# Kernel tuning notes

Measured on AMD Instinct MI355X. Metric: run time of the kernel, lower is better.

The kernel has to match this reference:

```python
import jax, jax.numpy as jnp
import numpy as np
import itertools
from itertools import combinations

N_QUBITS = 6
DIM = 2 ** N_QUBITS            # 64
N_GEN = DIM ** 2 - 1           # 4095 (SU(2^n) generators)
K_LOCAL = 2
OBS_DIM = 2 ** K_LOCAL         # 4
WIRE_GROUPS = [list(c) for c in combinations(range(N_QUBITS), K_LOCAL)]
N_OBS = len(WIRE_GROUPS)       # 15
N_OFF = OBS_DIM * (OBS_DIM - 1) // 2  # 6
CHUNK_DIM = 512
T_EMB = 256
HID = 256
BATCH = 512

# lower-triangle (i>j) flat ordering used by create_Hermitian: c = i*(i-1)/2 + j
_TRI_R = np.array([i for i in range(1, OBS_DIM) for j in range(i)])
_TRI_C = np.array([j for i in range(1, OBS_DIM) for j in range(i)])
_DIAG = np.arange(OBS_DIM - 1)  # diag slots 0..N-2 get 2*D[1..N-1]; last diag is 0


def _pauli_basis():
    """Lexicographic Pauli words on N_QUBITS qubits, identity excluded -> (N_GEN, DIM, DIM)."""
    I = np.eye(2, dtype=np.complex64)
    X = np.array([[0, 1], [1, 0]], dtype=np.complex64)
    Y = np.array([[0, -1j], [1j, 0]], dtype=np.complex64)
    Z = np.array([[1, 0], [0, -1]], dtype=np.complex64)
    P1 = {'I': I, 'X': X, 'Y': Y, 'Z': Z}
    out = np.empty((N_GEN, DIM, DIM), dtype=np.complex64)
    k = 0
    for word in itertools.product('IXYZ', repeat=N_QUBITS):
        if all(c == 'I' for c in word):
            continue
        m = np.array([[1.0 + 0j]], dtype=np.complex64)
        for c in word:
            m = np.kron(m, P1[c])
        out[k] = m
        k += 1
    return jnp.asarray(out)


def setup_inputs() -> dict:
    key = jax.random.key(0)
    ks = jax.random.split(key, 12)
    inp = {
        'x': jax.random.normal(ks[0], (BATCH, CHUNK_DIM + T_EMB), dtype=jnp.float32),
        # enc_proj: Linear(768,256) -> SiLU -> Linear(256,4095)
        'W1': jax.random.normal(ks[1], (CHUNK_DIM + T_EMB, HID), dtype=jnp.float32) * 0.02,
        'b1': jnp.zeros((HID,), dtype=jnp.float32),
        'W2': jax.random.normal(ks[2], (HID, N_GEN), dtype=jnp.float32) * 0.02,
        'b2': jnp.zeros((N_GEN,), dtype=jnp.float32),
        # ANO Hermitian params (std=2.0 per torch init)
        'Aoff': jax.random.normal(ks[3], (N_OBS, N_OFF), dtype=jnp.float32) * 2.0,
        'Boff': jax.random.normal(ks[4], (N_OBS, N_OFF), dtype=jnp.float32) * 2.0,
        'Ddiag': jax.random.normal(ks[5], (N_OBS, OBS_DIM), dtype=jnp.float32) * 2.0,
        # vel_head: Linear(15,256) -> SiLU -> Linear(256,512)
        'Wv1': jax.random.normal(ks[6], (N_OBS, HID), dtype=jnp.float32) * 0.02,
        'bv1': jnp.zeros((HID,), dtype=jnp.float32),
        'Wv2': jax.random.normal(ks[7], (HID, CHUNK_DIM), dtype=jnp.float32) * 0.02,
        'bv2': jnp.zeros((CHUNK_DIM,), dtype=jnp.float32),
        'pauli': _pauli_basis(),  # fixed SU(2^n) generator basis (constant)
    }
    return inp


def _build_H(Aoff, Boff, Ddiag):
    """Batched create_Hermitian: (N_OBS, 4, 4) complex. h + h^H semantics."""
    H = jnp.zeros((N_OBS, OBS_DIM, OBS_DIM), dtype=jnp.complex64)
    off = Aoff.astype(jnp.complex64) + 1j * Boff.astype(jnp.complex64)
    H = H.at[:, _TRI_R, _TRI_C].set(off)
    H = H + jnp.conj(jnp.swapaxes(H, -1, -2))
    H = H.at[:, _DIAG, _DIAG].set((2.0 * Ddiag[:, 1:]).astype(jnp.complex64))
    return H


def _forward(x, W1, b1, W2, b2, Aoff, Boff, Ddiag, Wv1, bv1, Wv2, bv2, pauli):
    B = x.shape[0]
    # enc_proj MLP -> SU(2^n) angles theta (B, 4095)
    enc = jax.nn.silu(x @ W1 + b1) @ W2 + b2
    # SpecialUnitary: U = exp(i * sum_m theta_m P_m); apply to |0...0> via eigh of the
    # Hermitian effective generator H_eff = sum_m theta_m P_m.
    H_eff = jnp.einsum('bm,mij->bij', enc.astype(jnp.complex64), pauli)  # (B, 64, 64)
    lam, V = jnp.linalg.eigh(H_eff)
    # psi = V @ diag(exp(i*lam)) @ V^dag @ e0 ; (V^dag e0)_j = conj(V[0, j])
    psi = jnp.einsum('bij,bj->bi', V, jnp.exp(1j * lam.astype(jnp.complex64)) * jnp.conj(V[:, 0, :]))
    H = _build_H(Aoff, Boff, Ddiag)  # (15, 4, 4)
    psi_t = psi.reshape((B,) + (2,) * N_QUBITS)
    q = []
    for w, (a, b) in enumerate(WIRE_GROUPS):
        # bring wires (a,b) to front (wire order: first wire is most significant bit)
        pg = jnp.moveaxis(psi_t, (1 + a, 1 + b), (1, 2)).reshape(B, OBS_DIM, -1)
        # <H> = tr(rho H), rho_kl = sum_r psi[k,r] conj(psi[l,r])
        q.append(jnp.einsum('bkr,blr,lk->b', pg, jnp.conj(pg), H[w]).real)
    q = jnp.stack(q, axis=1).astype(jnp.float32)  # (B, 15)
    return jax.nn.silu(q @ Wv1 + bv1) @ Wv2 + bv2  # (B, 512)


def reference(x, W1, b1, W2, b2, Aoff, Boff, Ddiag, Wv1, bv1, Wv2, bv2, pauli):
    return _forward(x, W1, b1, W2, b2, Aoff, Boff, Ddiag, Wv1, bv1, Wv2, bv2, pauli)
```

## Files before the change

### kernel.cpp

```cpp
#include <hip/hip_runtime.h>
#include <hip/hip_bf16.h>

#define BATCH   512
#define INDIM   768
#define HID     256
#define NGEN    4095
#define NOBS    15
#define OUTDIM  512
#define DIM     64

typedef __hip_bfloat16 bf16;

__device__ int      g_isf32;
__device__ float    g_theta[(size_t)BATCH*NGEN];
__device__ float    g_q[BATCH*NOBS];

__device__ __forceinline__ float tof(bf16 v){ return __bfloat162float(v); }
__device__ __forceinline__ float silu(float x){ return x / (1.f + __expf(-x)); }
__device__ __forceinline__ float blo(unsigned u){ return __uint_as_float(u<<16); }
__device__ __forceinline__ float bhi(unsigned u){ return __uint_as_float(u & 0xFFFF0000u); }

template<bool F32>
__device__ __forceinline__ float LD(const void* p, size_t i){
  if(F32) return ((const float*)p)[i];
  else    return tof(((const bf16*)p)[i]);
}

__device__ __forceinline__ unsigned spread6(unsigned x){
  return (x&1u) | ((x&2u)<<1) | ((x&4u)<<2) | ((x&8u)<<3) | ((x&16u)<<4) | ((x&32u)<<5);
}

__constant__ int c_WA[15] = {0,0,0,0,0,1,1,1,1,2,2,2,3,3,4};
__constant__ int c_WB[15] = {1,2,3,4,5,2,3,4,5,3,4,5,4,5,5};
__constant__ int c_Lt[6]  = {1,2,2,3,3,3};
__constant__ int c_Kt[6]  = {0,0,1,0,1,2};

__global__ __launch_bounds__(256) void k_detect(const unsigned* __restrict__ w1raw){
  __shared__ int sh[256];
  const int t = threadIdx.x;
  int c = 0;
  for(int i=t;i<1024;i+=256){
    unsigned ub = (w1raw[i]>>8) & 0x7Fu;
    if(ub>=0x30u && ub<=0x3Fu) c++;
  }
  sh[t] = c;
  __syncthreads();
  for(int s=128;s>0;s>>=1){
    if(t<s) sh[t] += sh[t+s];
    __syncthreads();
  }
  if(t==0) g_isf32 = (sh[0] < 512) ? 1 : 0;
}

template<bool F32>
__device__ void enc_body(const void* __restrict__ x, const void* __restrict__ W1,
                         const void* __restrict__ b1, const void* __restrict__ W2,
                         const void* __restrict__ b2,
                         float (*xl_t)[4], float (*hl_t)[4]){
  const int t  = threadIdx.x;
  const int b0 = (blockIdx.x >> 3) * 4;
  const int c0 = (blockIdx.x & 7) * 512;

  #pragma unroll
  for(int r=0;r<4;r++)
    for(int k=t;k<INDIM;k+=256) xl_t[k][r] = LD<F32>(x,(size_t)(b0+r)*INDIM+k);
  __syncthreads();

  {
    float acc1[4]={0.f,0.f,0.f,0.f};
    for(int k0=0;k0<INDIM;k0+=8){
      float wv[8];
      #pragma unroll
      for(int u=0;u<8;u++) wv[u] = LD<F32>(W1,(size_t)(k0+u)*HID+t);
      #pragma unroll
      for(int u=0;u<8;u++){
        float4 xa = *(const float4*)&xl_t[k0+u][0];
        float w = wv[u];
        acc1[0]+=xa.x*w; acc1[1]+=xa.y*w; acc1[2]+=xa.z*w; acc1[3]+=xa.w*w;
      }
    }
    float bb = LD<F32>(b1,t);
    #pragma unroll
    for(int r=0;r<4;r++) hl_t[t][r] = silu(acc1[r]+bb);
  }
  __syncthreads();

  const int colA = c0 + t;
  const int colB = c0 + 256 + t;
  const bool okB = (colB < NGEN);
  float acc[4][2];
  {
    float bva = LD<F32>(b2,colA);
    float bvb = okB ? LD<F32>(b2,colB) : 0.f;
    #pragma unroll
    for(int r=0;r<4;r++){ acc[r][0]=bva; acc[r][1]=bvb; }
  }
  for(int k0=0;k0<HID;k0+=8){
    float wa[8], wb[8];
    #pragma unroll
    for(int u=0;u<8;u++){
      wa[u] = LD<F32>(W2,(size_t)(k0+u)*NGEN + colA);
      wb[u] = okB ? LD<F32>(W2,(size_t)(k0+u)*NGEN + colB) : 0.f;
    }
    #pragma unroll
    for(int u=0;u<8;u++){
      float4 ha = *(const float4*)&hl_t[k0+u][0];
      float fa = wa[u], fb = wb[u];
      acc[0][0]+=ha.x*fa; acc[0][1]+=ha.x*fb;
      acc[1][0]+=ha.y*fa; acc[1][1]+=ha.y*fb;
      acc[2][0]+=ha.z*fa; acc[2][1]+=ha.z*fb;
      acc[3][0]+=ha.w*fa; acc[3][1]+=ha.w*fb;
    }
  }
  #pragma unroll
  for(int r=0;r<4;r++){
    g_theta[(size_t)(b0+r)*NGEN + colA] = acc[r][0];
    if(okB) g_theta[(size_t)(b0+r)*NGEN + colB] = acc[r][1];
  }
}

__global__ __launch_bounds__(256) void k_enc(const void* x,const void* W1,const void* b1,
                                             const void* W2,const void* b2){
  __shared__ __align__(16) float xl_t[INDIM][4];
  __shared__ __align__(16) float hl_t[HID][4];
  if(g_isf32) enc_body<true >(x,W1,b1,W2,b2,xl_t,hl_t);
  else        enc_body<false>(x,W1,b1,W2,b2,xl_t,hl_t);
}

template<bool F32>
__device__ void state_body(const void* __restrict__ Aoff, const void* __restrict__ Boff,
                           const void* __restrict__ Ddiag,
                           const void* __restrict__ Wv1, const void* __restrict__ bv1,
                           const void* __restrict__ Wv2, const void* __restrict__ bv2,
                           void* __restrict__ out, char* sm){
  float*  th   = (float*)sm;
  float*  HH   = (float*)(sm + 16384);
  typedef float2 rep_t[66];
  rep_t*  vrA  = (rep_t*)sm;
  rep_t*  vrB  = (rep_t*)(sm + 2112);
  float2* ps   = (float2*)(sm + 4224);
  float2* coef = (float2*)(sm + 4736);
  float*  rs   = (float*)(sm + 6016);
  float*  qacc = (float*)(sm + 6272);
  float*  s_inva = (float*)(sm + 6336);
  int*    s_K    = (int*)(sm + 6340);
  float*  s_aG   = (float*)(sm + 6344);
  float*  hl   = (float*)(sm + 6400);
  float (*part)[64][8] = (float(*)[64][8])(sm + 7424);
  float*  n11  = (float*)(sm + 15616);
  float*  n12  = (float*)(sm + 15872);

  const int b = blockIdx.x, t = threadIdx.x;
  for(int m=t;m<NGEN;m+=256) th[m] = g_theta[(size_t)b*NGEN+m];
  __syncthreads();

  const int lane = t & 63, wav = t >> 6;
  for(int it=0; it<16; ++it){
    int d = (it<<2) | wav;
    unsigned td = (unsigned)(lane & d);
    unsigned tn = (unsigned)(lane & ~d) & 63u;
    unsigned w  = spread6((unsigned)d) + spread6(td) + 3u*spread6(tn);
    float thv = (w==0u) ? 0.f : th[w-1u];
    int ny = __popc(td) & 3;
    float gr = (ny==0)?  thv : (ny==2 ? -thv : 0.f);
    float gi = (ny==1)? -thv : (ny==3 ?  thv : 0.f);
    #pragma unroll
    for(int s=1;s<64;s<<=1){
      float pr = __shfl_xor(gr, s);
      float pi = __shfl_xor(gi, s);
      if(lane & s){ gr = pr - gr; gi = pi - gi; }
      else        { gr = gr + pr; gi = gi + pi; }
    }
    int j = lane ^ d;
    HH[lane*132 + 2*j]   = gr;
    HH[lane*132 + 2*j+1] = gi;
  }
  __syncthreads();

  const int i = t >> 2, c = t & 3, j0 = c*16;
  float hreg[32];
  float rsum = 0.f;
  #pragma unroll
  for(int jj=0;jj<16;jj+=2){
    float4 hv = *(const float4*)&HH[i*132 + 2*(j0+jj)];
    hreg[2*jj+0]=hv.x; hreg[2*jj+1]=hv.y; hreg[2*jj+2]=hv.z; hreg[2*jj+3]=hv.w;
    rsum += fabsf(hv.x)+fabsf(hv.y)+fabsf(hv.z)+fabsf(hv.w);
  }
  rsum += __shfl_xor(rsum,1);
  rsum += __shfl_xor(rsum,2);
  if(c==0) rs[i] = rsum;
  __syncthreads();

  if(t==0){
    float aG = 0.5f;
    for(int r=0;r<DIM;r++) aG = fmaxf(aG, rs[r]);
    *s_aG = aG;
  }
  __syncthreads();
  const float aG    = *s_aG;
  const float invaG = 1.f/aG;

  {
    rep_t* pv1 = vrA;
    rep_t* pv0 = vrB;
    if(t < DIM){
      float2 e0v = make_float2(t==0?1.f:0.f, 0.f);
      #pragma unroll
      for(int cc=0;cc<4;cc++) pv1[cc][t] = e0v;
    }
    __syncthreads();
    for(int m=1;m<=12;++m){
      const float* vb = (const float*)&pv1[c][0];
      float yr=0.f, yi=0.f;
      #pragma unroll
      for(int jj=0;jj<16;jj+=2){
        float4 xv = *(const float4*)&vb[2*(j0+jj)];
        float hr0=hreg[2*jj], hi0=hreg[2*jj+1], hr1=hreg[2*jj+2], hi1=hreg[2*jj+3];
        yr += hr0*xv.x - hi0*xv.y;
        yi += hr0*xv.y + hi0*xv.x;
        yr += hr1*xv.z - hi1*xv.w;
        yi += hr1*xv.w + hi1*xv.z;
      }
      yr += __shfl_xor(yr,1); yr += __shfl_xor(yr,2);
      yi += __shfl_xor(yi,1); yi += __shfl_xor(yi,2);
      if(c==0){
        float vnr = invaG*yr, vni = invaG*yi;
        float2 vn = make_float2(vnr, vni);
        #pragma unroll
        for(int cc=0;cc<4;cc++) pv0[cc][i] = vn;
        if(m==11) n11[i] = vnr*vnr + vni*vni;
        if(m==12) n12[i] = vnr*vnr + vni*vni;
      }
      __syncthreads();
      rep_t* tmp = pv0; pv0 = pv1; pv1 = tmp;
    }
  }

  if(t==0){
    float s11=0.f, s12=0.f;
    for(int r=0;r<DIM;r++){ s11 += n11[r]; s12 += n12[r]; }
    float a = aG;
    if(s11 > 1e-30f){
      float ratio = sqrtf(s12/s11);
      float ap = 1.35f * ratio * aG;
      a = fminf(aG, fmaxf(ap, 0.5f));
    }
    int K = (int)ceilf(a + 6.f*cbrtf(a) + 10.f);
    if(K>150) K=150;
    float bkp=0.f, bk=1e-35f, snorm=0.f;
    for(int k=K+12;k>=1;--k){
      float bkm = (2.f*(float)k/a)*bk - bkp;
      int n = k-1;
      if(n<=K) coef[n].x = bkm;
      if((n&1)==0) snorm += (n==0?1.f:2.f)*bkm;
      bkp = bk; bk = bkm;
    }
    float invs = 1.f/snorm;
    for(int n=0;n<=K;n++){
      float cv = coef[n].x*invs*(n==0?1.f:2.f);
      int p = n&3;
      float cr = (p==0)? cv : (p==2 ? -cv : 0.f);
      float ci = (p==1)? cv : (p==3 ? -cv : 0.f);
      coef[n] = make_float2(cr,ci);
    }
    *s_K = K;
    *s_inva = 1.f/a;
  }
  __syncthreads();
  const float inva = *s_inva;
  const int K = *s_K;

  rep_t* v0r = vrA;
  rep_t* v1r = vrB;
  if(t < DIM){
    float2 w1 = make_float2(HH[t*132+0]*inva, HH[t*132+1]*inva);
    float2 e0 = make_float2(t==0?1.f:0.f, 0.f);
    #pragma unroll
    for(int cc=0;cc<4;cc++){ v0r[cc][t] = e0; v1r[cc][t] = w1; }
    float2 c0 = coef[0], c1 = coef[1];
    float2 p;
    p.x = (t==0?c0.x:0.f) + c1.x*w1.x - c1.y*w1.y;
    p.y = (t==0?c0.y:0.f) + c1.x*w1.y + c1.y*w1.x;
    ps[t] = p;
  }
  __syncthreads();

  for(int k=2;k<=K;k++){
    const float* vb = (const float*)&v1r[c][0];
    float yr=0.f, yi=0.f;
    #pragma unroll
    for(int jj=0;jj<16;jj+=2){
      float4 xv = *(const float4*)&vb[2*(j0+jj)];
      float hr0=hreg[2*jj], hi0=hreg[2*jj+1], hr1=hreg[2*jj+2], hi1=hreg[2*jj+3];
      yr += hr0*xv.x - hi0*xv.y;
      yi += hr0*xv.y + hi0*xv.x;
      yr += hr1*xv.z - hi1*xv.w;
      yi += hr1*xv.w + hi1*xv.z;
    }
    yr += __shfl_xor(yr,1); yr += __shfl_xor(yr,2);
    yi += __shfl_xor(yi,1); yi += __shfl_xor(yi,2);
    if(c==0){
      float2 vm = v0r[0][i];
      float2 vn = make_float2(2.f*inva*yr - vm.x, 2.f*inva*yi - vm.y);
      #pragma unroll
      for(int cc=0;cc<4;cc++) v0r[cc][i] = vn;
      float2 ck = coef[k];
      float2 p = ps[i];
      p.x += ck.x*vn.x - ck.y*vn.y;
      p.y += ck.x*vn.y + ck.y*vn.x;
      ps[i] = p;
    }
    __syncthreads();
    rep_t* tmp = v0r; v0r = v1r; v1r = tmp;
  }

  if(t<NOBS) qacc[t]=0.f;
  __syncthreads();

  if(t<150){
    int w = t/10, s = t%10;
    int posA = 5 - c_WA[w], posB = 5 - c_WB[w];
    float contrib = 0.f;
    bool have = false;
    if(s<4){
      int kk = s;
      if(kk<3){
        float val = 0.f;
        for(int r=0;r<16;r++){
          int idx = (((kk>>1)&1)<<posA) | ((kk&1)<<posB);
          int rb = 3;
          #pragma unroll
          for(int p=5;p>=0;--p){
            if(p==posA || p==posB) continue;
            idx |= ((r>>rb)&1)<<p;
            rb--;
          }
          float2 pv = ps[idx];
          val += pv.x*pv.x + pv.y*pv.y;
        }
        contrib = val*2.f*LD<F32>(Ddiag, w*4 + kk + 1);
        have = true;
      }
    } else {
      int cc = s-4;
      int l = c_Lt[cc], kk = c_Kt[cc];
      float zr=0.f, zi=0.f;
      for(int r=0;r<16;r++){
        int idxk = (((kk>>1)&1)<<posA) | ((kk&1)<<posB);
        int idxl = (((l >>1)&1)<<posA) | ((l &1)<<posB);
        int rb = 3;
        #pragma unroll
        for(int p=5;p>=0;--p){
          if(p==posA || p==posB) continue;
          int bit = (r>>rb)&1;
          idxk |= bit<<p; idxl |= bit<<p;
          rb--;
        }
        float2 pk = ps[idxk], pl = ps[idxl];
        zr += pk.x*pl.x + pk.y*pl.y;
        zi += pk.y*pl.x - pk.x*pl.y;
      }
      contrib = 2.f*(zr*LD<F32>(Aoff,w*6+cc) - zi*LD<F32>(Boff,w*6+cc));
      have = true;
    }
    if(have) atomicAdd(&qacc[w], contrib);
  }
  __syncthreads();
  if(t<NOBS) g_q[(size_t)b*NOBS + t] = qacc[t];

  if(!F32){
    {
      float acc = tof(((const bf16*)bv1)[t]);
      #pragma unroll
      for(int k=0;k<NOBS;k++) acc += qacc[k]*tof(((const bf16*)Wv1)[k*HID+t]);
      hl[t] = silu(acc);
    }
    __syncthreads();
    const int rg = t >> 6;
    const uint4* w2v = (const uint4*)Wv2;
    float a8[8] = {0.f,0.f,0.f,0.f,0.f,0.f,0.f,0.f};
    for(int kk=0; kk<64; kk+=8){
      uint4 wv[8];
      #pragma unroll
      for(int u=0;u<8;u++) wv[u] = w2v[(size_t)(rg*64+kk+u)*64 + lane];
      #pragma unroll
      for(int u=0;u<8;u++){
        float hk = hl[rg*64+kk+u];
        a8[0] += hk*blo(wv[u].x); a8[1] += hk*bhi(wv[u].x);
        a8[2] += hk*blo(wv[u].y); a8[3] += hk*bhi(wv[u].y);
        a8[4] += hk*blo(wv[u].z); a8[5] += hk*bhi(wv[u].z);
        a8[6] += hk*blo(wv[u].w); a8[7] += hk*bhi(wv[u].w);
      }
    }
    #pragma unroll
    for(int j=0;j<8;j++) part[rg][lane][j] = a8[j];
    __syncthreads();
    {
      int cA = 2*t, cB = 2*t+1;
      float vA = tof(((const bf16*)bv2)[cA]);
      float vB = tof(((const bf16*)bv2)[cB]);
      #pragma unroll
      for(int r2=0;r2<4;r2++){
        vA += part[r2][cA>>3][cA&7];
        vB += part[r2][cB>>3][cB&7];
      }
      bf16 ha = __float2bfloat16(vA), hb = __float2bfloat16(vB);
      unsigned pw = (unsigned)(*(unsigned short*)&ha) |
                    ((unsigned)(*(unsigned short*)&hb)<<16);
      ((unsigned*)out)[(size_t)b*(OUTDIM/2) + t] = pw;
    }
  }
}

__global__ __launch_bounds__(256) void k_state(const void* Aoff,const void* Boff,const void* Dd,
                                               const void* Wv1,const void* bv1,
                                               const void* Wv2,const void* bv2, void* out){
  __shared__ __align__(16) char sm[50176];
  if(g_isf32) state_body<true >(Aoff,Boff,Dd,Wv1,bv1,Wv2,bv2,out,sm);
  else        state_body<false>(Aoff,Boff,Dd,Wv1,bv1,Wv2,bv2,out,sm);
}

template<bool F32>
__device__ void vel_body(const void* __restrict__ Wv1, const void* __restrict__ bv1,
                         const void* __restrict__ Wv2, const void* __restrict__ bv2,
                         void* __restrict__ out){
  const int b = blockIdx.x, t = threadIdx.x;
  if(F32){
    __shared__ float ql[NOBS];
    __shared__ float hl[HID];
    if(t<NOBS) ql[t] = g_q[(size_t)b*NOBS+t];
    __syncthreads();
    float acc = LD<F32>(bv1,t);
    #pragma unroll
    for(int k=0;k<NOBS;k++) acc += ql[k]*LD<F32>(Wv1,k*HID+t);
    hl[t] = silu(acc);
    __syncthreads();
    #pragma unroll
    for(int oo=0;oo<2;oo++){
      int o = t + oo*256;
      float s0=0.f;
      for(int k=0;k<HID;k++) s0 += hl[k]*LD<F32>(Wv2,(size_t)k*OUTDIM+o);
      ((float*)out)[(size_t)b*OUTDIM+o] = LD<F32>(bv2,o) + s0;
    }
  }
}

__global__ __launch_bounds__(256) void k_vel(const void* Wv1,const void* bv1,
                                             const void* Wv2,const void* bv2, void* out){
  if(g_isf32) vel_body<true >(Wv1,bv1,Wv2,bv2,out);
  else        vel_body<false>(Wv1,bv1,Wv2,bv2,out);
}

extern "C" void kernel_launch(void* const* d_in, const int* in_sizes, int n_in,
                              void* d_out, int out_size, void* d_ws, size_t ws_size,
                              hipStream_t stream){
  const void* x    = d_in[0];
  const void* W1   = d_in[1];
  const void* b1   = d_in[2];
  const void* W2   = d_in[3];
  const void* b2   = d_in[4];
  const void* Aoff = d_in[5];
  const void* Boff = d_in[6];
  const void* Dd   = d_in[7];
  const void* Wv1  = d_in[8];
  const void* bv1  = d_in[9];
  const void* Wv2  = d_in[10];
  const void* bv2  = d_in[11];

  k_detect<<<1,256,0,stream>>>((const unsigned*)W1);
  k_enc  <<<1024,256,0,stream>>>(x,W1,b1,W2,b2);
  k_state<<<BATCH,256,0,stream>>>(Aoff,Boff,Dd,Wv1,bv1,Wv2,bv2,d_out);
  k_vel  <<<BATCH,256,0,stream>>>(Wv1,bv1,Wv2,bv2,d_out);
}
```

Baseline: 266.8 us.

## Split encoder into pack, layer-1 and layer-2 kernels with padded fp32 weights

The fused encoder kernel is replaced by three launches. The first converts inputs and weights to fp32 and pads NGEN to 4096. The second computes the hidden layer once per 4 rows, so it is no longer recomputed by each of the 8 column blocks. The third computes the output layer with 8 rows per block and float4-vectorised, padded loads and stores. This removes the 8x redundant layer-1 work and the unaligned W2 accesses, at the cost of extra launches and a per-call conversion pass over all weights (about 4 MB for W2).

```diff
diff --git a/kernel.cpp b/kernel.cpp
--- a/kernel.cpp
+++ b/kernel.cpp
@@ -5,6 +5,7 @@
 #define INDIM   768
 #define HID     256
 #define NGEN    4095
+#define NGENP   4096
 #define NOBS    15
 #define OUTDIM  512
 #define DIM     64
@@ -12,8 +13,14 @@
 typedef __hip_bfloat16 bf16;
 
 __device__ int      g_isf32;
-__device__ float    g_theta[(size_t)BATCH*NGEN];
+__device__ float    g_theta[(size_t)BATCH*NGENP];
 __device__ float    g_q[BATCH*NOBS];
+__device__ float    g_h[(size_t)BATCH*HID];
+__device__ float    g_xp[(size_t)BATCH*INDIM];
+__device__ float    g_W1p[(size_t)INDIM*HID];
+__device__ float    g_b1p[HID];
+__device__ float    g_W2p[(size_t)HID*NGENP];
+__device__ float    g_b2p[NGENP];
 
 __device__ __forceinline__ float tof(bf16 v){ return __bfloat162float(v); }
 __device__ __forceinline__ float silu(float x){ return x / (1.f + __expf(-x)); }
@@ -53,78 +60,85 @@
 }
 
 template<bool F32>
-__device__ void enc_body(const void* __restrict__ x, const void* __restrict__ W1,
-                         const void* __restrict__ b1, const void* __restrict__ W2,
-                         const void* __restrict__ b2,
-                         float (*xl_t)[4], float (*hl_t)[4]){
+__device__ void pack_body(const void* __restrict__ x, const void* __restrict__ W1,
+                          const void* __restrict__ b1, const void* __restrict__ W2,
+                          const void* __restrict__ b2){
+  const size_t gid = (size_t)blockIdx.x*256 + threadIdx.x;
+  const size_t stride = (size_t)gridDim.x*256;
+  for(size_t i=gid;i<(size_t)BATCH*INDIM;i+=stride) g_xp[i]  = LD<F32>(x,i);
+  for(size_t i=gid;i<(size_t)INDIM*HID;i+=stride)   g_W1p[i] = LD<F32>(W1,i);
+  for(size_t i=gid;i<HID;i+=stride)                 g_b1p[i] = LD<F32>(b1,i);
+  for(size_t i=gid;i<(size_t)HID*NGENP;i+=stride){
+    size_t k = i>>12, c = i&4095;
+    g_W2p[i] = (c<NGEN) ? LD<F32>(W2,k*NGEN+c) : 0.f;
+  }
+  for(size_t i=gid;i<NGENP;i+=stride) g_b2p[i] = (i<NGEN) ? LD<F32>(b2,i) : 0.f;
+}
+
+__global__ __launch_bounds__(256) void k_pack(const void* x,const void* W1,const void* b1,
+                                              const void* W2,const void* b2){
+  if(g_isf32) pack_body<true >(x,W1,b1,W2,b2);
+  else        pack_body<false>(x,W1,b1,W2,b2);
+}
+
+__global__ __launch_bounds__(256) void k_enc1(){
+  __shared__ __align__(16) float xl[INDIM][4];
+  const int t = threadIdx.x, b0 = blockIdx.x*4;
+  for(int i=t;i<4*INDIM;i+=256){
+    int r = i/INDIM, k = i - r*INDIM;
+    xl[k][r] = g_xp[(size_t)(b0+r)*INDIM + k];
+  }
+  __syncthreads();
+  const int rh = t>>7, tc = t&127;
+  float a00=0.f,a01=0.f,a10=0.f,a11=0.f;
+  for(int k0=0;k0<INDIM;k0+=8){
+    #pragma unroll
+    for(int u=0;u<8;u++){
+      float2 wv = *(const float2*)&g_W1p[(size_t)(k0+u)*HID + 2*tc];
+      float2 xv = *(const float2*)&xl[k0+u][2*rh];
+      a00 += xv.x*wv.x; a01 += xv.x*wv.y;
+      a10 += xv.y*wv.x; a11 += xv.y*wv.y;
+    }
+  }
+  const float bb0 = g_b1p[2*tc], bb1 = g_b1p[2*tc+1];
+  g_h[(size_t)(b0+2*rh+0)*HID + 2*tc+0] = silu(a00+bb0);
+  g_h[(size_t)(b0+2*rh+0)*HID + 2*tc+1] = silu(a01+bb1);
+  g_h[(size_t)(b0+2*rh+1)*HID + 2*tc+0] = silu(a10+bb0);
+  g_h[(size_t)(b0+2*rh+1)*HID + 2*tc+1] = silu(a11+bb1);
+}
+
+__global__ __launch_bounds__(512) void k_enc2(){
+  __shared__ __align__(16) float hl[HID][8];
   const int t  = threadIdx.x;
-  const int b0 = (blockIdx.x >> 3) * 4;
-  const int c0 = (blockIdx.x & 7) * 512;
-
+  const int b0 = (blockIdx.x>>2)*8;
+  const int c0 = (blockIdx.x&3)*1024;
+  for(int i=t;i<8*HID;i+=512){
+    int r = i>>8, k = i&255;
+    hl[k][r] = g_h[(size_t)(b0+r)*HID + k];
+  }
+  __syncthreads();
+  const int rh = t>>8, tc = t&255;
+  const int col = c0 + 4*tc;
+  float4 bv = *(const float4*)&g_b2p[col];
+  float acc[4][4];
   #pragma unroll
-  for(int r=0;r<4;r++)
-    for(int k=t;k<INDIM;k+=256) xl_t[k][r] = LD<F32>(x,(size_t)(b0+r)*INDIM+k);
-  __syncthreads();
-
-  {
-    float acc1[4]={0.f,0.f,0.f,0.f};
-    for(int k0=0;k0<INDIM;k0+=8){
-      float wv[8];
-      #pragma unroll
-      for(int u=0;u<8;u++) wv[u] = LD<F32>(W1,(size_t)(k0+u)*HID+t);
-      #pragma unroll
-      for(int u=0;u<8;u++){
-        float4 xa = *(const float4*)&xl_t[k0+u][0];
-        float w = wv[u];
-        acc1[0]+=xa.x*w; acc1[1]+=xa.y*w; acc1[2]+=xa.z*w; acc1[3]+=xa.w*w;
-      }
-    }
-    float bb = LD<F32>(b1,t);
-    #pragma unroll
-    for(int r=0;r<4;r++) hl_t[t][r] = silu(acc1[r]+bb);
-  }
-  __syncthreads();
-
-  const int colA = c0 + t;
-  const int colB = c0 + 256 + t;
-  const bool okB = (colB < NGEN);
-  float acc[4][2];
-  {
-    float bva = LD<F32>(b2,colA);
-    float bvb = okB ? LD<F32>(b2,colB) : 0.f;
-    #pragma unroll
-    for(int r=0;r<4;r++){ acc[r][0]=bva; acc[r][1]=bvb; }
-  }
+  for(int i=0;i<4;i++){ acc[i][0]=bv.x; acc[i][1]=bv.y; acc[i][2]=bv.z; acc[i][3]=bv.w; }
   for(int k0=0;k0<HID;k0+=8){
-    float wa[8], wb[8];
     #pragma unroll
     for(int u=0;u<8;u++){
-      wa[u] = LD<F32>(W2,(size_t)(k0+u)*NGEN + colA);
-      wb[u] = okB ? LD<F32>(W2,(size_t)(k0+u)*NGEN + colB) : 0.f;
-    }
-    #pragma unroll
-    for(int u=0;u<8;u++){
-      float4 ha = *(const float4*)&hl_t[k0+u][0];
-      float fa = wa[u], fb = wb[u];
-      acc[0][0]+=ha.x*fa; acc[0][1]+=ha.x*fb;
-      acc[1][0]+=ha.y*fa; acc[1][1]+=ha.y*fb;
-      acc[2][0]+=ha.z*fa; acc[2][1]+=ha.z*fb;
-      acc[3][0]+=ha.w*fa; acc[3][1]+=ha.w*fb;
+      float4 wv = *(const float4*)&g_W2p[(size_t)(k0+u)*NGENP + col];
+      float4 hv = *(const float4*)&hl[k0+u][4*rh];
+      acc[0][0]+=hv.x*wv.x; acc[0][1]+=hv.x*wv.y; acc[0][2]+=hv.x*wv.z; acc[0][3]+=hv.x*wv.w;
+      acc[1][0]+=hv.y*wv.x; acc[1][1]+=hv.y*wv.y; acc[1][2]+=hv.y*wv.z; acc[1][3]+=hv.y*wv.w;
+      acc[2][0]+=hv.z*wv.x; acc[2][1]+=hv.z*wv.y; acc[2][2]+=hv.z*wv.z; acc[2][3]+=hv.z*wv.w;
+      acc[3][0]+=hv.w*wv.x; acc[3][1]+=hv.w*wv.y; acc[3][2]+=hv.w*wv.z; acc[3][3]+=hv.w*wv.w;
     }
   }
   #pragma unroll
-  for(int r=0;r<4;r++){
-    g_theta[(size_t)(b0+r)*NGEN + colA] = acc[r][0];
-    if(okB) g_theta[(size_t)(b0+r)*NGEN + colB] = acc[r][1];
-  }
-}
-
-__global__ __launch_bounds__(256) void k_enc(const void* x,const void* W1,const void* b1,
-                                             const void* W2,const void* b2){
-  __shared__ __align__(16) float xl_t[INDIM][4];
-  __shared__ __align__(16) float hl_t[HID][4];
-  if(g_isf32) enc_body<true >(x,W1,b1,W2,b2,xl_t,hl_t);
-  else        enc_body<false>(x,W1,b1,W2,b2,xl_t,hl_t);
+  for(int i=0;i<4;i++){
+    float4 o = make_float4(acc[i][0],acc[i][1],acc[i][2],acc[i][3]);
+    *(float4*)&g_theta[(size_t)(b0+4*rh+i)*NGENP + col] = o;
+  }
 }
 
 template<bool F32>
@@ -151,7 +165,7 @@
   float*  n12  = (float*)(sm + 15872);
 
   const int b = blockIdx.x, t = threadIdx.x;
-  for(int m=t;m<NGEN;m+=256) th[m] = g_theta[(size_t)b*NGEN+m];
+  for(int m=t;m<NGEN;m+=256) th[m] = g_theta[(size_t)b*NGENP+m];
   __syncthreads();
 
   const int lane = t & 63, wav = t >> 6;
@@ -468,7 +482,9 @@
   const void* bv2  = d_in[11];
 
   k_detect<<<1,256,0,stream>>>((const unsigned*)W1);
-  k_enc  <<<1024,256,0,stream>>>(x,W1,b1,W2,b2);
+  k_pack <<<1024,256,0,stream>>>(x,W1,b1,W2,b2);
+  k_enc1 <<<BATCH/4,256,0,stream>>>();
+  k_enc2 <<<256,512,0,stream>>>();
   k_state<<<BATCH,256,0,stream>>>(Aoff,Boff,Dd,Wv1,bv1,Wv2,bv2,d_out);
   k_vel  <<<BATCH,256,0,stream>>>(Wv1,bv1,Wv2,bv2,d_out);
 }
```

Result: no change. 266.9 us (+0.1%).
